# Kernel optimization log

Hardware: AMD Instinct MI355X
Metric: run time of the kernel (lower is better)

The kernel has to match this reference:

```python
import jax, jax.numpy as jnp
import numpy as np

ALIGNED_H = 7
ALIGNED_W = 7
IMG_H, IMG_W = 800.0, 1216.0


def setup_inputs() -> dict:
    key = jax.random.key(0)
    k1, k2, k3, k4 = jax.random.split(key, 4)
    N, C, H, W = 2, 256, 200, 304
    R = 2000
    features = jax.random.normal(k1, (N, C, H, W), dtype=jnp.float32)
    # rois: [batch_idx, x1, y1, x2, y2] in image coordinates
    bidx = jax.random.randint(k2, (R,), 0, N).astype(jnp.float32)
    xy1 = jax.random.uniform(k3, (R, 2)) * jnp.array([IMG_W * 0.7, IMG_H * 0.7])
    wh = 16.0 + jax.random.uniform(k4, (R, 2)) * jnp.array([IMG_W * 0.3 - 16.0, IMG_H * 0.3 - 16.0])
    xy2 = jnp.minimum(xy1 + wh, jnp.array([IMG_W - 1.0, IMG_H - 1.0]))
    rois = jnp.concatenate([bidx[:, None], xy1[:, 0:1], xy1[:, 1:2], xy2[:, 0:1], xy2[:, 1:2]], axis=1).astype(jnp.float32)
    spatial_scale = jnp.float32(0.25)
    return {"features": features, "rois": rois, "spatial_scale": spatial_scale}


def roi_align(features, rois, spatial_scale, ah, aw):
    N, C, H, W = features.shape
    b = rois[:, 0].astype(jnp.int32)                       # [R]
    x1 = rois[:, 1] * spatial_scale
    y1 = rois[:, 2] * spatial_scale
    x2 = rois[:, 3] * spatial_scale
    y2 = rois[:, 4] * spatial_scale
    roi_w = jnp.maximum(x2 - x1 + 1.0, 0.0)
    roi_h = jnp.maximum(y2 - y1 + 1.0, 0.0)
    bin_h = roi_h / (ah - 1.0)                             # [R]
    bin_w = roi_w / (aw - 1.0)
    ph = jnp.arange(ah, dtype=jnp.float32)
    pw = jnp.arange(aw, dtype=jnp.float32)
    h = y1[:, None] + ph[None, :] * bin_h[:, None]         # [R, ah]
    w = x1[:, None] + pw[None, :] * bin_w[:, None]         # [R, aw]
    valid = ((h >= 0) & (h < H))[:, :, None] & ((w >= 0) & (w < W))[:, None, :]  # [R, ah, aw]
    hs = jnp.clip(jnp.floor(h), 0.0, H - 2.0)              # kernel: min(floor(h), H-2)
    ws = jnp.clip(jnp.floor(w), 0.0, W - 2.0)
    dh = (h - hs)[:, :, None]                              # [R, ah, 1]
    dw = (w - ws)[:, None, :]                              # [R, 1, aw]
    yi = hs.astype(jnp.int32)[:, :, None]                  # [R, ah, 1]
    xi = ws.astype(jnp.int32)[:, None, :]                  # [R, 1, aw]
    bi = b[:, None, None]                                  # [R, 1, 1]
    # gather 4 corners -> [R, ah, aw, C]
    v00 = features[bi, :, yi, xi]
    v01 = features[bi, :, yi, xi + 1]
    v10 = features[bi, :, yi + 1, xi]
    v11 = features[bi, :, yi + 1, xi + 1]
    dh4 = dh[..., None]
    dw4 = dw[..., None]
    val = (v00 * (1 - dh4) * (1 - dw4) + v01 * (1 - dh4) * dw4
           + v10 * dh4 * (1 - dw4) + v11 * dh4 * dw4)
    out = jnp.where(valid[..., None], val, 0.0)            # [R, ah, aw, C]
    return jnp.transpose(out, (0, 3, 1, 2))                # [R, C, ah, aw]


def reference(features, rois, spatial_scale):
    return roi_align(features, rois, spatial_scale, ALIGNED_H, ALIGNED_W)
```

## Files before the change

kernel.cpp:

```cpp
#include <hip/hip_runtime.h>
#include <hip/hip_bf16.h>

#define C_ 256
#define H_ 200
#define W_ 304
#define AH 7
#define AW 7
#define KK (AH * AW)
#define SP 260

typedef float f32x4 __attribute__((ext_vector_type(4)));

__device__ __forceinline__ float b2f(unsigned short s) {
    return __uint_as_float((unsigned int)s << 16);
}

__global__ __launch_bounds__(256) void transpose_nchw_nhwc_bf16(
    const float* __restrict__ in, unsigned short* __restrict__ out) {
    __shared__ unsigned int tile[128][34];
    const int HW = H_ * W_;
    const int n  = blockIdx.z;
    const int p0 = blockIdx.x * 64;
    const int c0 = blockIdx.y * 128;
    const float* inb = in + (size_t)n * C_ * HW;
    unsigned short* outb = out + (size_t)n * HW * C_;

    {
        const int q  = threadIdx.x & 15;
        const int r0 = threadIdx.x >> 4;
        #pragma unroll
        for (int i = 0; i < 8; ++i) {
            const int c = r0 + 16 * i;
            const f32x4 v = __builtin_nontemporal_load(
                (const f32x4*)&inb[(size_t)(c0 + c) * HW + p0 + 4 * q]);
            const __hip_bfloat162 lo = __float22bfloat162_rn(make_float2(v.x, v.y));
            const __hip_bfloat162 hi = __float22bfloat162_rn(make_float2(v.z, v.w));
            unsigned int ulo, uhi;
            __builtin_memcpy(&ulo, &lo, 4);
            __builtin_memcpy(&uhi, &hi, 4);
            *(uint2*)&tile[c][2 * q] = make_uint2(ulo, uhi);
        }
    }
    __syncthreads();
    {
        const int pp0 = threadIdx.x & 15;
        const int cq  = threadIdx.x >> 4;
        #pragma unroll
        for (int i = 0; i < 2; ++i) {
            const int pp = pp0 + 16 * i;
            unsigned int u[8];
            #pragma unroll
            for (int j = 0; j < 8; ++j) u[j] = tile[8 * cq + j][pp];
            unsigned int pe[4], po[4];
            #pragma unroll
            for (int k = 0; k < 4; ++k) {
                pe[k] = (u[2 * k] & 0xFFFFu) | (u[2 * k + 1] << 16);
                po[k] = (u[2 * k] >> 16) | (u[2 * k + 1] & 0xFFFF0000u);
            }
            unsigned short* oA = &outb[(size_t)(p0 + 2 * pp) * C_ + c0 + 8 * cq];
            unsigned short* oB = oA + C_;
            *(uint4*)oA = make_uint4(pe[0], pe[1], pe[2], pe[3]);
            *(uint4*)oB = make_uint4(po[0], po[1], po[2], po[3]);
        }
    }
}

__global__ __launch_bounds__(512) void roialign_nhwc_bf16(
    const unsigned short* __restrict__ tf, const float* __restrict__ rois,
    const float* __restrict__ scale_ptr, float* __restrict__ out) {
    __shared__ float sout[KK * SP];
    const int r    = blockIdx.x;
    const int wave = threadIdx.x >> 6;
    const int lane = threadIdx.x & 63;
    const int c4   = lane * 4;

    const float scale = scale_ptr[0];
    const float* roi = rois + (size_t)r * 5;
    const int   b  = (int)roi[0];
    const float x1 = roi[1] * scale;
    const float y1 = roi[2] * scale;
    const float x2 = roi[3] * scale;
    const float y2 = roi[4] * scale;
    const float roi_w = fmaxf(x2 - x1 + 1.0f, 0.0f);
    const float roi_h = fmaxf(y2 - y1 + 1.0f, 0.0f);
    const float bin_h = roi_h / (float)(AH - 1);
    const float bin_w = roi_w / (float)(AW - 1);
    const unsigned short* fb = tf + (size_t)b * (H_ * W_) * C_;

    #pragma unroll 2
    for (int k = wave; k < KK; k += 8) {
        const int ph = k / AW;
        const int pw = k - ph * AW;
        const float h  = y1 + (float)ph * bin_h;
        const float w  = x1 + (float)pw * bin_w;
        const float hs = fminf(fmaxf(floorf(h), 0.0f), (float)(H_ - 2));
        const float ws = fminf(fmaxf(floorf(w), 0.0f), (float)(W_ - 2));
        const float dh = h - hs;
        const float dw = w - ws;
        const int   yi = (int)hs;
        const int   xi = (int)ws;
        const bool  valid = (h >= 0.0f) && (h < (float)H_) &&
                            (w >= 0.0f) && (w < (float)W_);
        const unsigned short* p = fb + ((size_t)yi * W_ + xi) * C_ + c4;
        const ushort4 a00 = *(const ushort4*)p;
        const ushort4 a01 = *(const ushort4*)(p + C_);
        const ushort4 a10 = *(const ushort4*)(p + (size_t)W_ * C_);
        const ushort4 a11 = *(const ushort4*)(p + (size_t)W_ * C_ + C_);
        const float w00 = (1.0f - dh) * (1.0f - dw);
        const float w01 = (1.0f - dh) * dw;
        const float w10 = dh * (1.0f - dw);
        const float w11 = dh * dw;
        float4 v;
        v.x = b2f(a00.x) * w00 + b2f(a01.x) * w01 + b2f(a10.x) * w10 + b2f(a11.x) * w11;
        v.y = b2f(a00.y) * w00 + b2f(a01.y) * w01 + b2f(a10.y) * w10 + b2f(a11.y) * w11;
        v.z = b2f(a00.z) * w00 + b2f(a01.z) * w01 + b2f(a10.z) * w10 + b2f(a11.z) * w11;
        v.w = b2f(a00.w) * w00 + b2f(a01.w) * w01 + b2f(a10.w) * w10 + b2f(a11.w) * w11;
        if (!valid) { v.x = 0.0f; v.y = 0.0f; v.z = 0.0f; v.w = 0.0f; }
        *(float4*)&sout[k * SP + c4] = v;
    }
    __syncthreads();
    float* ob = out + (size_t)r * C_ * KK;
    const int nf4 = C_ * KK / 4;
    for (int idx = threadIdx.x; idx < nf4; idx += 512) {
        const int f = 4 * idx;
        f32x4 v;
        #pragma unroll
        for (int e = 0; e < 4; ++e) {
            const int fe = f + e;
            const int c = fe / KK;
            const int k = fe - c * KK;
            v[e] = sout[k * SP + c];
        }
        __builtin_nontemporal_store(v, (f32x4*)&ob[f]);
    }
}

__global__ __launch_bounds__(256) void roialign_nchw(
    const float* __restrict__ feat, const float* __restrict__ rois,
    const float* __restrict__ scale_ptr, float* __restrict__ out) {
    __shared__ float sout[C_ * KK];
    const int r = blockIdx.x;
    const int c = threadIdx.x;
    const float scale = scale_ptr[0];
    const float* roi = rois + (size_t)r * 5;
    const int   b  = (int)roi[0];
    const float x1 = roi[1] * scale;
    const float y1 = roi[2] * scale;
    const float x2 = roi[3] * scale;
    const float y2 = roi[4] * scale;
    const float roi_w = fmaxf(x2 - x1 + 1.0f, 0.0f);
    const float roi_h = fmaxf(y2 - y1 + 1.0f, 0.0f);
    const float bin_h = roi_h / (float)(AH - 1);
    const float bin_w = roi_w / (float)(AW - 1);
    const float* fb = feat + ((size_t)b * C_ + c) * (H_ * W_);

    for (int ph = 0; ph < AH; ++ph) {
        const float h  = y1 + (float)ph * bin_h;
        const float hs = fminf(fmaxf(floorf(h), 0.0f), (float)(H_ - 2));
        const float dh = h - hs;
        const int   yi = (int)hs;
        const bool  vh = (h >= 0.0f) && (h < (float)H_);
        #pragma unroll
        for (int pw = 0; pw < AW; ++pw) {
            const float w  = x1 + (float)pw * bin_w;
            const float ws = fminf(fmaxf(floorf(w), 0.0f), (float)(W_ - 2));
            const float dw = w - ws;
            const int   xi = (int)ws;
            const bool  valid = vh && (w >= 0.0f) && (w < (float)W_);
            const float v00 = fb[(size_t)yi * W_ + xi];
            const float v01 = fb[(size_t)yi * W_ + xi + 1];
            const float v10 = fb[(size_t)(yi + 1) * W_ + xi];
            const float v11 = fb[(size_t)(yi + 1) * W_ + xi + 1];
            float val = v00 * (1.0f - dh) * (1.0f - dw)
                      + v01 * (1.0f - dh) * dw
                      + v10 * dh * (1.0f - dw)
                      + v11 * dh * dw;
            sout[c * KK + ph * AW + pw] = valid ? val : 0.0f;
        }
    }
    __syncthreads();
    float* ob = out + (size_t)r * C_ * KK;
    #pragma unroll 4
    for (int i = threadIdx.x; i < C_ * KK; i += 256) ob[i] = sout[i];
}

extern "C" void kernel_launch(void* const* d_in, const int* in_sizes, int n_in,
                              void* d_out, int out_size, void* d_ws, size_t ws_size,
                              hipStream_t stream) {
    const float* feat  = (const float*)d_in[0];
    const float* rois  = (const float*)d_in[1];
    const float* scale = (const float*)d_in[2];
    float* out = (float*)d_out;

    const int R = in_sizes[1] / 5;
    const int N = in_sizes[0] / (C_ * H_ * W_);
    const size_t need = (size_t)N * C_ * H_ * W_ * sizeof(unsigned short);

    if (ws_size >= need) {
        unsigned short* tf = (unsigned short*)d_ws;
        dim3 tb(256);
        dim3 tg((H_ * W_) / 64, C_ / 128, N);
        hipLaunchKernelGGL(transpose_nchw_nhwc_bf16, tg, tb, 0, stream, feat, tf);
        hipLaunchKernelGGL(roialign_nhwc_bf16, dim3(R), dim3(512), 0, stream,
                           tf, rois, scale, out);
    } else {
        hipLaunchKernelGGL(roialign_nchw, dim3(R), dim3(256), 0, stream,
                           feat, rois, scale, out);
    }
}
```

Before: 79.23 us.

## Switch to fp16 staging and a compact fp16 shared tile for ROI output transpose

Switches the transposed feature copy from bf16 to fp16. The ROI kernel now keeps its per-ROI output tile in shared memory as fp16, in channel-major order padded to 66, instead of an fp32 tile in bin-major order. Each wave computes fixed pairs of bins, and a new write-out loop turns 8 contiguous bins per thread into unaligned vector stores. This cuts shared memory use per block so more blocks can be resident, and removes the division-heavy index arithmetic in the store loop. In exchange it rounds the interpolated results to fp16 a second time, and an fp16 overflow on large inputs is a precision risk.

```diff
diff --git a/kernel.cpp b/kernel.cpp
--- a/kernel.cpp
+++ b/kernel.cpp
@@ -1,21 +1,24 @@
 #include <hip/hip_runtime.h>
-#include <hip/hip_bf16.h>
 
 #define C_ 256
 #define H_ 200
 #define W_ 304
 #define AH 7
 #define AW 7
-#define KK (AH * AW)
-#define SP 260
-
-typedef float f32x4 __attribute__((ext_vector_type(4)));
-
-__device__ __forceinline__ float b2f(unsigned short s) {
-    return __uint_as_float((unsigned int)s << 16);
-}
-
-__global__ __launch_bounds__(256) void transpose_nchw_nhwc_bf16(
+#define KK 49
+#define PADK 66
+
+typedef float f32x4  __attribute__((ext_vector_type(4)));
+typedef float f32x4u __attribute__((ext_vector_type(4), aligned(4)));
+
+__device__ __forceinline__ float h2f(unsigned short s) {
+    _Float16 h; __builtin_memcpy(&h, &s, 2); return (float)h;
+}
+__device__ __forceinline__ unsigned short f2h(float f) {
+    _Float16 h = (_Float16)f; unsigned short s; __builtin_memcpy(&s, &h, 2); return s;
+}
+
+__global__ __launch_bounds__(256) void transpose_nchw_nhwc_f16(
     const float* __restrict__ in, unsigned short* __restrict__ out) {
     __shared__ unsigned int tile[128][34];
     const int HW = H_ * W_;
@@ -33,11 +36,8 @@
             const int c = r0 + 16 * i;
             const f32x4 v = __builtin_nontemporal_load(
                 (const f32x4*)&inb[(size_t)(c0 + c) * HW + p0 + 4 * q]);
-            const __hip_bfloat162 lo = __float22bfloat162_rn(make_float2(v.x, v.y));
-            const __hip_bfloat162 hi = __float22bfloat162_rn(make_float2(v.z, v.w));
-            unsigned int ulo, uhi;
-            __builtin_memcpy(&ulo, &lo, 4);
-            __builtin_memcpy(&uhi, &hi, 4);
+            const unsigned int ulo = (unsigned)f2h(v.x) | ((unsigned)f2h(v.y) << 16);
+            const unsigned int uhi = (unsigned)f2h(v.z) | ((unsigned)f2h(v.w) << 16);
             *(uint2*)&tile[c][2 * q] = make_uint2(ulo, uhi);
         }
     }
@@ -50,7 +50,7 @@
             const int pp = pp0 + 16 * i;
             unsigned int u[8];
             #pragma unroll
-            for (int j = 0; j < 8; ++j) u[j] = tile[8 * cq + j][pp];
+            for (int jj = 0; jj < 8; ++jj) u[jj] = tile[8 * cq + jj][pp];
             unsigned int pe[4], po[4];
             #pragma unroll
             for (int k = 0; k < 4; ++k) {
@@ -65,10 +65,41 @@
     }
 }
 
-__global__ __launch_bounds__(512) void roialign_nhwc_bf16(
+__device__ __forceinline__ void samp(
+    const unsigned short* __restrict__ fb, int k,
+    float y1, float x1, float bin_h, float bin_w, int c4, float* o) {
+    const int ph = k / AW;
+    const int pw = k - ph * AW;
+    const float h  = y1 + (float)ph * bin_h;
+    const float w  = x1 + (float)pw * bin_w;
+    const float hs = fminf(fmaxf(floorf(h), 0.0f), (float)(H_ - 2));
+    const float ws = fminf(fmaxf(floorf(w), 0.0f), (float)(W_ - 2));
+    const float dh = h - hs;
+    const float dw = w - ws;
+    const int   yi = (int)hs;
+    const int   xi = (int)ws;
+    const bool  valid = (h >= 0.0f) && (h < (float)H_) &&
+                        (w >= 0.0f) && (w < (float)W_);
+    const unsigned short* p = fb + ((size_t)yi * W_ + xi) * C_ + c4;
+    const ushort4 a00 = *(const ushort4*)p;
+    const ushort4 a01 = *(const ushort4*)(p + C_);
+    const ushort4 a10 = *(const ushort4*)(p + (size_t)W_ * C_);
+    const ushort4 a11 = *(const ushort4*)(p + (size_t)W_ * C_ + C_);
+    const float w00 = (1.0f - dh) * (1.0f - dw);
+    const float w01 = (1.0f - dh) * dw;
+    const float w10 = dh * (1.0f - dw);
+    const float w11 = dh * dw;
+    o[0] = h2f(a00.x) * w00 + h2f(a01.x) * w01 + h2f(a10.x) * w10 + h2f(a11.x) * w11;
+    o[1] = h2f(a00.y) * w00 + h2f(a01.y) * w01 + h2f(a10.y) * w10 + h2f(a11.y) * w11;
+    o[2] = h2f(a00.z) * w00 + h2f(a01.z) * w01 + h2f(a10.z) * w10 + h2f(a11.z) * w11;
+    o[3] = h2f(a00.w) * w00 + h2f(a01.w) * w01 + h2f(a10.w) * w10 + h2f(a11.w) * w11;
+    if (!valid) { o[0] = 0.0f; o[1] = 0.0f; o[2] = 0.0f; o[3] = 0.0f; }
+}
+
+__global__ __launch_bounds__(512, 6) void roialign_nhwc_f16(
     const unsigned short* __restrict__ tf, const float* __restrict__ rois,
     const float* __restrict__ scale_ptr, float* __restrict__ out) {
-    __shared__ float sout[KK * SP];
+    __shared__ unsigned short sh[C_ * PADK];
     const int r    = blockIdx.x;
     const int wave = threadIdx.x >> 6;
     const int lane = threadIdx.x & 63;
@@ -87,51 +118,50 @@
     const float bin_w = roi_w / (float)(AW - 1);
     const unsigned short* fb = tf + (size_t)b * (H_ * W_) * C_;
 
-    #pragma unroll 2
-    for (int k = wave; k < KK; k += 8) {
-        const int ph = k / AW;
-        const int pw = k - ph * AW;
-        const float h  = y1 + (float)ph * bin_h;
-        const float w  = x1 + (float)pw * bin_w;
-        const float hs = fminf(fmaxf(floorf(h), 0.0f), (float)(H_ - 2));
-        const float ws = fminf(fmaxf(floorf(w), 0.0f), (float)(W_ - 2));
-        const float dh = h - hs;
-        const float dw = w - ws;
-        const int   yi = (int)hs;
-        const int   xi = (int)ws;
-        const bool  valid = (h >= 0.0f) && (h < (float)H_) &&
-                            (w >= 0.0f) && (w < (float)W_);
-        const unsigned short* p = fb + ((size_t)yi * W_ + xi) * C_ + c4;
-        const ushort4 a00 = *(const ushort4*)p;
-        const ushort4 a01 = *(const ushort4*)(p + C_);
-        const ushort4 a10 = *(const ushort4*)(p + (size_t)W_ * C_);
-        const ushort4 a11 = *(const ushort4*)(p + (size_t)W_ * C_ + C_);
-        const float w00 = (1.0f - dh) * (1.0f - dw);
-        const float w01 = (1.0f - dh) * dw;
-        const float w10 = dh * (1.0f - dw);
-        const float w11 = dh * dw;
-        float4 v;
-        v.x = b2f(a00.x) * w00 + b2f(a01.x) * w01 + b2f(a10.x) * w10 + b2f(a11.x) * w11;
-        v.y = b2f(a00.y) * w00 + b2f(a01.y) * w01 + b2f(a10.y) * w10 + b2f(a11.y) * w11;
-        v.z = b2f(a00.z) * w00 + b2f(a01.z) * w01 + b2f(a10.z) * w10 + b2f(a11.z) * w11;
-        v.w = b2f(a00.w) * w00 + b2f(a01.w) * w01 + b2f(a10.w) * w10 + b2f(a11.w) * w11;
-        if (!valid) { v.x = 0.0f; v.y = 0.0f; v.z = 0.0f; v.w = 0.0f; }
-        *(float4*)&sout[k * SP + c4] = v;
+    for (int kp = 3 * wave; kp < 3 * wave + 3; ++kp) {
+        const int kA = 2 * kp;
+        float vA[4], vB[4];
+        samp(fb, kA,     y1, x1, bin_h, bin_w, c4, vA);
+        samp(fb, kA + 1, y1, x1, bin_h, bin_w, c4, vB);
+        #pragma unroll
+        for (int j = 0; j < 4; ++j) {
+            const unsigned int u = (unsigned)f2h(vA[j]) | ((unsigned)f2h(vB[j]) << 16);
+            *(unsigned int*)&sh[(c4 + j) * PADK + kA] = u;
+        }
+    }
+    if (wave == 7) {
+        float v[4];
+        samp(fb, 48, y1, x1, bin_h, bin_w, c4, v);
+        #pragma unroll
+        for (int j = 0; j < 4; ++j) sh[(c4 + j) * PADK + 48] = f2h(v[j]);
     }
     __syncthreads();
-    float* ob = out + (size_t)r * C_ * KK;
-    const int nf4 = C_ * KK / 4;
-    for (int idx = threadIdx.x; idx < nf4; idx += 512) {
-        const int f = 4 * idx;
-        f32x4 v;
-        #pragma unroll
-        for (int e = 0; e < 4; ++e) {
-            const int fe = f + e;
-            const int c = fe / KK;
-            const int k = fe - c * KK;
-            v[e] = sout[k * SP + c];
-        }
-        __builtin_nontemporal_store(v, (f32x4*)&ob[f]);
+
+    const int j  = threadIdx.x & 7;
+    const int cs = threadIdx.x >> 3;
+    float* ob = out + (size_t)r * (C_ * KK);
+    if (j < 7) {
+        #pragma unroll
+        for (int it = 0; it < 4; ++it) {
+            const int c = cs + 64 * it;
+            const unsigned short* row = &sh[c * PADK + 8 * j];
+            float f[8];
+            #pragma unroll
+            for (int e = 0; e < 4; ++e) {
+                const unsigned int u = *(const unsigned int*)&row[2 * e];
+                f[2 * e]     = h2f((unsigned short)(u & 0xFFFFu));
+                f[2 * e + 1] = h2f((unsigned short)(u >> 16));
+            }
+            float* dst = &ob[c * KK + 8 * j];
+            if (j < 6) {
+                f32x4u a = { f[0], f[1], f[2], f[3] };
+                f32x4u bb = { f[4], f[5], f[6], f[7] };
+                __builtin_nontemporal_store(a, (f32x4u*)dst);
+                __builtin_nontemporal_store(bb, (f32x4u*)(dst + 4));
+            } else {
+                __builtin_nontemporal_store(f[0], dst);
+            }
+        }
     }
 }
 
@@ -200,8 +230,8 @@
         unsigned short* tf = (unsigned short*)d_ws;
         dim3 tb(256);
         dim3 tg((H_ * W_) / 64, C_ / 128, N);
-        hipLaunchKernelGGL(transpose_nchw_nhwc_bf16, tg, tb, 0, stream, feat, tf);
-        hipLaunchKernelGGL(roialign_nhwc_bf16, dim3(R), dim3(512), 0, stream,
+        hipLaunchKernelGGL(transpose_nchw_nhwc_f16, tg, tb, 0, stream, feat, tf);
+        hipLaunchKernelGGL(roialign_nhwc_f16, dim3(R), dim3(512), 0, stream,
                            tf, rois, scale, out);
     } else {
         hipLaunchKernelGGL(roialign_nchw, dim3(R), dim3(256), 0, stream,
```

After: 94.43 us. +19.2%, slower.
